# Performance work log

Measured on AMD Instinct MI355X. Metric: run time of the kernel, lower is better.

The kernel has to match this reference:

```python
import jax, jax.numpy as jnp
import numpy as np

KERNEL_SIZE = 7
DILATION = 1
DYNAMIC_SIZE = 3


def setup_inputs() -> dict:
    key = jax.random.key(0)
    # [B, 2*(channels+1), H, W]; channels = 8 filterable + (8+2) param channels
    x = jax.random.normal(key, (2, 18, 1024, 1024), dtype=jnp.float32)
    return {"input": x}


def _bilateral(filterable, params, kernel_size, dilation):
    # filterable: [B, C, H, W]; params: [B, C+2, H, W] (already negated squares)
    B, C, H, W = filterable.shape
    r = kernel_size // 2
    pad = r * dilation
    fp = jnp.pad(filterable, ((0, 0), (0, 0), (pad, pad), (pad, pad)))
    mp = jnp.pad(jnp.ones((B, 1, H, W), filterable.dtype),
                 ((0, 0), (0, 0), (pad, pad), (pad, pad)))  # validity mask
    range_p = params[:, :C]      # per-channel range coefficients (<= 0)
    sx = params[:, C]            # spatial x coefficient (<= 0)
    sy = params[:, C + 1]        # spatial y coefficient (<= 0)
    acc = jnp.zeros_like(filterable)
    wsum = jnp.zeros((B, H, W), filterable.dtype)
    for i in range(kernel_size):        # fixed small window: loop is structural
        for j in range(kernel_size):
            oy, ox = i * dilation, j * dilation
            fn = jax.lax.dynamic_slice(fp, (0, 0, oy, ox), (B, C, H, W))
            m = jax.lax.dynamic_slice(mp, (0, 0, oy, ox), (B, 1, H, W))[:, 0]
            d2 = (fn - filterable) ** 2
            dy2 = float(((i - r) * dilation) ** 2)
            dx2 = float(((j - r) * dilation) ** 2)
            logw = jnp.einsum('bchw,bchw->bhw', range_p, d2) + sx * dx2 + sy * dy2
            w = jnp.exp(logw) * m   # out-of-bounds taps masked to 0
            acc = acc + w[:, None] * fn
            wsum = wsum + w
    # center tap has weight exp(0)=1, so wsum >= 1 (no div-by-zero)
    return acc / wsum[:, None]


def reference(input):
    C_in = input.shape[1]
    channels = C_in // 2 - 1
    filterable = input[:, :channels]
    params = input[:, channels:]
    params = -(params * params)
    filtered = _bilateral(filterable, params, KERNEL_SIZE, DILATION)
    return filtered[:, :DYNAMIC_SIZE]
```

## Files before the change

kernel.cpp:

```cpp
#include <hip/hip_runtime.h>

namespace {

constexpr int H = 1024;
constexpr int W = 1024;
constexpr int PLANE = H * W;
constexpr int CIN = 18;
constexpr int C = 8;
constexpr int TX = 16;
constexpr int TY = 16;
constexpr int SW = TX + 6;
constexpr int SH = TY + 6;
constexpr int PSTR = 9;
constexpr int ROWF = SW * PSTR;

template<bool INTERIOR>
__device__ __forceinline__ void run_tile(const float* __restrict__ inb,
                                         float* __restrict__ outb,
                                         float* lds,
                                         int gy0, int gx0)
{
    const int tx = threadIdx.x, ty = threadIdx.y;
    const int tid = ty * TX + tx;

    constexpr int TOT = SH * C * SW;
    for (int idx = tid; idx < TOT; idx += TX * TY) {
        int y = idx / (C * SW);
        int rem = idx - y * (C * SW);
        int c = rem / SW;
        int x = rem - c * SW;
        int gy = gy0 + y - 3;
        int gx = gx0 + x - 3;
        float v = 0.0f;
        if (INTERIOR || ((unsigned)gy < (unsigned)H && (unsigned)gx < (unsigned)W))
            v = inb[c * PLANE + gy * W + gx];
        lds[y * ROWF + x * PSTR + c] = v;
    }
    if (!INTERIOR) {
        for (int idx = tid; idx < SH * SW; idx += TX * TY) {
            int y = idx / SW;
            int x = idx - y * SW;
            int gy = gy0 + y - 3;
            int gx = gx0 + x - 3;
            lds[y * ROWF + x * PSTR + C] =
                ((unsigned)gy < (unsigned)H && (unsigned)gx < (unsigned)W) ? 1.0f : 0.0f;
        }
    }
    __syncthreads();

    const int gy = gy0 + ty, gx = gx0 + tx;
    const int pofs = gy * W + gx;
    const float* lp = lds + ty * ROWF + tx * PSTR;

    float f[C];
#pragma unroll
    for (int c = 0; c < C; ++c) f[c] = lp[3 * ROWF + 3 * PSTR + c];

    float rp[C];
#pragma unroll
    for (int c = 0; c < C; ++c) {
        float p = inb[(C + c) * PLANE + pofs];
        rp[c] = -(p * p);
    }
    float px_ = inb[16 * PLANE + pofs];
    float py_ = inb[17 * PLANE + pofs];
    const float sx = -(px_ * px_);
    const float sy = -(py_ * py_);

    float acc0 = 0.f, acc1 = 0.f, acc2 = 0.f, ws = 0.f;
#pragma unroll
    for (int i = 0; i < 7; ++i) {
        const float ey = sy * (float)((i - 3) * (i - 3));
#pragma unroll
        for (int j = 0; j < 7; ++j) {
            const float* q = lp + (i * ROWF + j * PSTR);
            float logw = fmaf(sx, (float)((j - 3) * (j - 3)), ey);
            float fn0 = q[0], fn1 = q[1], fn2 = q[2], fn3 = q[3];
            float fn4 = q[4], fn5 = q[5], fn6 = q[6], fn7 = q[7];
            float d;
            d = fn0 - f[0]; logw = fmaf(rp[0] * d, d, logw);
            d = fn1 - f[1]; logw = fmaf(rp[1] * d, d, logw);
            d = fn2 - f[2]; logw = fmaf(rp[2] * d, d, logw);
            d = fn3 - f[3]; logw = fmaf(rp[3] * d, d, logw);
            d = fn4 - f[4]; logw = fmaf(rp[4] * d, d, logw);
            d = fn5 - f[5]; logw = fmaf(rp[5] * d, d, logw);
            d = fn6 - f[6]; logw = fmaf(rp[6] * d, d, logw);
            d = fn7 - f[7]; logw = fmaf(rp[7] * d, d, logw);
            float w = __expf(logw);
            if (!INTERIOR) w *= q[C];
            ws += w;
            acc0 = fmaf(w, fn0, acc0);
            acc1 = fmaf(w, fn1, acc1);
            acc2 = fmaf(w, fn2, acc2);
        }
    }
    const float inv = 1.0f / ws;
    outb[pofs]             = acc0 * inv;
    outb[PLANE + pofs]     = acc1 * inv;
    outb[2 * PLANE + pofs] = acc2 * inv;
}

__global__ __launch_bounds__(TX * TY, 4) void bilateral_kernel(const float* __restrict__ in,
                                                               float* __restrict__ out)
{
    __shared__ float lds[SH * ROWF];
    const int b = blockIdx.z;
    const int gx0 = blockIdx.x * TX;
    const int gy0 = blockIdx.y * TY;
    const float* inb = in + (size_t)b * CIN * PLANE;
    float* outb = out + (size_t)b * 3 * PLANE;

    const bool interior = (gx0 >= 3) && (gx0 + TX + 3 <= W) &&
                          (gy0 >= 3) && (gy0 + TY + 3 <= H);
    if (interior)
        run_tile<true>(inb, outb, lds, gy0, gx0);
    else
        run_tile<false>(inb, outb, lds, gy0, gx0);
}

}

extern "C" void kernel_launch(void* const* d_in, const int* in_sizes, int n_in,
                              void* d_out, int out_size, void* d_ws, size_t ws_size,
                              hipStream_t stream)
{
    const float* in = (const float*)d_in[0];
    float* out = (float*)d_out;
    dim3 grid(W / TX, H / TY, 2);
    dim3 block(TX, TY);
    hipLaunchKernelGGL(bilateral_kernel, grid, block, 0, stream, in, out);
}
```

Baseline: 289.4 us.

## Store tile in fp16 and compute range weights with packed dot2

The LDS tile now holds the 8 filterable channels as one packed half8 vector per position, with a separate float mask array. Range distances are computed with packed fp16 subtract and multiply, then accumulated with fdot2 against fp16 range coefficients. The exponent is pre-scaled by log2(e) so the native exp2 instruction can be used. This cuts LDS traffic and VALU work per tap, at the cost of fp16 rounding on the inputs and the distance terms, which may hurt accuracy.

```diff
diff --git a/kernel.cpp b/kernel.cpp
--- a/kernel.cpp
+++ b/kernel.cpp
@@ -11,87 +11,117 @@
 constexpr int TY = 16;
 constexpr int SW = TX + 6;
 constexpr int SH = TY + 6;
-constexpr int PSTR = 9;
-constexpr int ROWF = SW * PSTR;
+constexpr int NPOS = SW * SH;
+constexpr float LOG2E = 1.44269504088896340736f;
+
+typedef _Float16 half2_t __attribute__((ext_vector_type(2)));
+typedef _Float16 half8_t __attribute__((ext_vector_type(8)));
+
+__device__ __forceinline__ float dot2acc(half2_t a, half2_t b, float c) {
+#if defined(__has_builtin)
+#if __has_builtin(__builtin_amdgcn_fdot2)
+    return __builtin_amdgcn_fdot2(a, b, c, false);
+#else
+    return fmaf((float)a[0], (float)b[0], fmaf((float)a[1], (float)b[1], c));
+#endif
+#else
+    return fmaf((float)a[0], (float)b[0], fmaf((float)a[1], (float)b[1], c));
+#endif
+}
+
+__device__ __forceinline__ float fast_exp2(float x) {
+#if defined(__has_builtin)
+#if __has_builtin(__builtin_amdgcn_exp2f)
+    return __builtin_amdgcn_exp2f(x);
+#else
+    return exp2f(x);
+#endif
+#else
+    return exp2f(x);
+#endif
+}
 
 template<bool INTERIOR>
 __device__ __forceinline__ void run_tile(const float* __restrict__ inb,
                                          float* __restrict__ outb,
-                                         float* lds,
+                                         half8_t* __restrict__ tile,
+                                         float* __restrict__ msk,
                                          int gy0, int gx0)
 {
     const int tx = threadIdx.x, ty = threadIdx.y;
     const int tid = ty * TX + tx;
 
-    constexpr int TOT = SH * C * SW;
-    for (int idx = tid; idx < TOT; idx += TX * TY) {
-        int y = idx / (C * SW);
-        int rem = idx - y * (C * SW);
-        int c = rem / SW;
-        int x = rem - c * SW;
+    for (int idx = tid; idx < NPOS; idx += TX * TY) {
+        int y = idx / SW;
+        int x = idx - y * SW;
         int gy = gy0 + y - 3;
         int gx = gx0 + x - 3;
-        float v = 0.0f;
-        if (INTERIOR || ((unsigned)gy < (unsigned)H && (unsigned)gx < (unsigned)W))
-            v = inb[c * PLANE + gy * W + gx];
-        lds[y * ROWF + x * PSTR + c] = v;
-    }
-    if (!INTERIOR) {
-        for (int idx = tid; idx < SH * SW; idx += TX * TY) {
-            int y = idx / SW;
-            int x = idx - y * SW;
-            int gy = gy0 + y - 3;
-            int gx = gx0 + x - 3;
-            lds[y * ROWF + x * PSTR + C] =
-                ((unsigned)gy < (unsigned)H && (unsigned)gx < (unsigned)W) ? 1.0f : 0.0f;
+        half8_t hv;
+        if (INTERIOR || ((unsigned)gy < (unsigned)H && (unsigned)gx < (unsigned)W)) {
+            const float* p = inb + gy * W + gx;
+#pragma unroll
+            for (int c = 0; c < C; ++c) hv[c] = (_Float16)p[c * PLANE];
+            if (!INTERIOR) msk[idx] = 1.0f;
+        } else {
+#pragma unroll
+            for (int c = 0; c < C; ++c) hv[c] = (_Float16)0.0f;
+            msk[idx] = 0.0f;
         }
+        tile[idx] = hv;
     }
     __syncthreads();
 
     const int gy = gy0 + ty, gx = gx0 + tx;
     const int pofs = gy * W + gx;
-    const float* lp = lds + ty * ROWF + tx * PSTR;
+    const half8_t* lp = tile + ty * SW + tx;
 
-    float f[C];
+    const half8_t fc = lp[3 * SW + 3];
+
+    half2_t rp01, rp23, rp45, rp67;
+    {
+        const float* pp = inb + C * PLANE + pofs;
+        float r[C];
 #pragma unroll
-    for (int c = 0; c < C; ++c) f[c] = lp[3 * ROWF + 3 * PSTR + c];
-
-    float rp[C];
-#pragma unroll
-    for (int c = 0; c < C; ++c) {
-        float p = inb[(C + c) * PLANE + pofs];
-        rp[c] = -(p * p);
+        for (int c = 0; c < C; ++c) {
+            float p = pp[c * PLANE];
+            r[c] = -(p * p) * LOG2E;
+        }
+        rp01 = half2_t{(_Float16)r[0], (_Float16)r[1]};
+        rp23 = half2_t{(_Float16)r[2], (_Float16)r[3]};
+        rp45 = half2_t{(_Float16)r[4], (_Float16)r[5]};
+        rp67 = half2_t{(_Float16)r[6], (_Float16)r[7]};
     }
     float px_ = inb[16 * PLANE + pofs];
     float py_ = inb[17 * PLANE + pofs];
-    const float sx = -(px_ * px_);
-    const float sy = -(py_ * py_);
+    const float sx = -(px_ * px_) * LOG2E;
+    const float sy = -(py_ * py_) * LOG2E;
+
+    float exj[7];
+#pragma unroll
+    for (int j = 0; j < 7; ++j) exj[j] = sx * (float)((j - 3) * (j - 3));
 
     float acc0 = 0.f, acc1 = 0.f, acc2 = 0.f, ws = 0.f;
 #pragma unroll
     for (int i = 0; i < 7; ++i) {
         const float ey = sy * (float)((i - 3) * (i - 3));
+        const half8_t* row = lp + i * SW;
+        const float* mrow = msk + (ty + i) * SW + tx;
 #pragma unroll
         for (int j = 0; j < 7; ++j) {
-            const float* q = lp + (i * ROWF + j * PSTR);
-            float logw = fmaf(sx, (float)((j - 3) * (j - 3)), ey);
-            float fn0 = q[0], fn1 = q[1], fn2 = q[2], fn3 = q[3];
-            float fn4 = q[4], fn5 = q[5], fn6 = q[6], fn7 = q[7];
-            float d;
-            d = fn0 - f[0]; logw = fmaf(rp[0] * d, d, logw);
-            d = fn1 - f[1]; logw = fmaf(rp[1] * d, d, logw);
-            d = fn2 - f[2]; logw = fmaf(rp[2] * d, d, logw);
-            d = fn3 - f[3]; logw = fmaf(rp[3] * d, d, logw);
-            d = fn4 - f[4]; logw = fmaf(rp[4] * d, d, logw);
-            d = fn5 - f[5]; logw = fmaf(rp[5] * d, d, logw);
-            d = fn6 - f[6]; logw = fmaf(rp[6] * d, d, logw);
-            d = fn7 - f[7]; logw = fmaf(rp[7] * d, d, logw);
-            float w = __expf(logw);
-            if (!INTERIOR) w *= q[C];
+            half8_t q = row[j];
+            half8_t d = q - fc;
+            half8_t dd = d * d;
+            float logw = exj[j] + ey;
+            logw = dot2acc(__builtin_shufflevector(dd, dd, 0, 1), rp01, logw);
+            logw = dot2acc(__builtin_shufflevector(dd, dd, 2, 3), rp23, logw);
+            logw = dot2acc(__builtin_shufflevector(dd, dd, 4, 5), rp45, logw);
+            logw = dot2acc(__builtin_shufflevector(dd, dd, 6, 7), rp67, logw);
+            float w = fast_exp2(logw);
+            if (!INTERIOR) w *= mrow[j];
             ws += w;
-            acc0 = fmaf(w, fn0, acc0);
-            acc1 = fmaf(w, fn1, acc1);
-            acc2 = fmaf(w, fn2, acc2);
+            acc0 = fmaf(w, (float)q[0], acc0);
+            acc1 = fmaf(w, (float)q[1], acc1);
+            acc2 = fmaf(w, (float)q[2], acc2);
         }
     }
     const float inv = 1.0f / ws;
@@ -103,7 +133,8 @@
 __global__ __launch_bounds__(TX * TY, 4) void bilateral_kernel(const float* __restrict__ in,
                                                                float* __restrict__ out)
 {
-    __shared__ float lds[SH * ROWF];
+    __shared__ __align__(16) half8_t tile[NPOS];
+    __shared__ float msk[NPOS];
     const int b = blockIdx.z;
     const int gx0 = blockIdx.x * TX;
     const int gy0 = blockIdx.y * TY;
@@ -113,9 +144,9 @@
     const bool interior = (gx0 >= 3) && (gx0 + TX + 3 <= W) &&
                           (gy0 >= 3) && (gy0 + TY + 3 <= H);
     if (interior)
-        run_tile<true>(inb, outb, lds, gy0, gx0);
+        run_tile<true>(inb, outb, tile, msk, gy0, gx0);
     else
-        run_tile<false>(inb, outb, lds, gy0, gx0);
+        run_tile<false>(inb, outb, tile, msk, gy0, gx0);
 }
 
 }
```

New measurement: 254.9 us. 11.9% less time.
